# Kernel tuning notes

Hardware: AMD Instinct MI355X
Metric: run time of the kernel (lower is better)

The kernel has to match this reference:

```python
import jax, jax.numpy as jnp
import numpy as np


def setup_inputs() -> dict:
    key = jax.random.key(0)
    kx, kw = jax.random.split(key)
    x = jax.random.normal(kx, (32, 64, 112, 112), dtype=jnp.float32)
    weights = jax.random.normal(kw, (128, 64, 3, 3), dtype=jnp.float32)
    return {"x": x, "weights": weights}


def reference(x, weights):
    # The torch module's triple loop computes a standard VALID conv2d,
    # stride 1, no padding, weights shared across spatial locations.
    # x: [B, Cin, H, W]; weights: [Cout, Cin, k, k] -> out: [B, Cout, H-k+1, W-k+1]
    out = jax.lax.conv_general_dilated(
        x, weights,
        window_strides=(1, 1),
        padding="VALID",
        dimension_numbers=("NCHW", "OIHW", "NCHW"),
    )
    return out
```

## Files before the change

kernel.cpp:

```cpp
#include <hip/hip_runtime.h>


typedef short bf16x8 __attribute__((ext_vector_type(8)));
typedef float f32x4 __attribute__((ext_vector_type(4)));

__device__ __forceinline__ unsigned short f2bf(float f) {
    unsigned int u = __builtin_bit_cast(unsigned int, f);
    unsigned int r = u + 0x7fffu + ((u >> 16) & 1u);
    return (unsigned short)(r >> 16);
}
__device__ __forceinline__ unsigned int pack2(float lo, float hi) {
    return (unsigned)f2bf(lo) | ((unsigned)f2bf(hi) << 16);
}

__global__ void wperm_kernel(const float* __restrict__ W, unsigned short* __restrict__ wp) {
    int t = blockIdx.x * 256 + threadIdx.x;
    if (t < 73728) {
        int r  = t >> 13;
        int co = (t >> 6) & 127;
        int ci = t & 63;
        wp[t] = f2bf(W[(co * 64 + ci) * 9 + r]);
    }
}

__global__ __launch_bounds__(256, 2) void conv_mfma(const float* __restrict__ x,
                                                    const unsigned short* __restrict__ wp,
                                                    float* __restrict__ out) {
    __shared__ alignas(16) unsigned short xwin[324 * 72];
    __shared__ alignas(16) unsigned short wpl[128 * 72];

    const int tid  = threadIdx.x;
    const int lane = tid & 63;
    const int wv   = tid >> 6;
    const int quad = lane >> 4;
    const int l15  = lane & 15;

    const int blk  = blockIdx.x;
    const int xcd  = blk & 7;
    const int slot = blk >> 3;
    const int b    = xcd + 8 * (slot / 49);
    const int tile = slot % 49;
    const int oh0  = (tile / 7) * 16;
    const int ow0  = (tile % 7) * 16;

    const float* xb = x + b * 802816;

    const uint4* wsrc = reinterpret_cast<const uint4*>(wp) + tid * 4;
    uint4 wreg[4];
    #pragma unroll
    for (int j = 0; j < 4; j++) wreg[j] = wsrc[j];

    for (int t = tid; t < 2304; t += 256) {
        const int cgl = t & 7;
        const int hwl = (t >> 3) & 7;
        const int cgh = (t >> 6) & 3;
        const int hwh = t >> 8;
        const int cg  = cgh * 8 + cgl;
        const int hw  = hwh * 8 + hwl;
        const int hh  = hw >> 2;
        const int wc  = hw & 3;
        const int h   = min(oh0 + hh, 111);
        const float* p0 = xb + (2 * cg) * 12544 + h * 112 + ow0 + wc * 4;
        const f32x4 a = *reinterpret_cast<const f32x4*>(p0);
        const f32x4 c = *reinterpret_cast<const f32x4*>(p0 + 12544);
        unsigned int* dst = reinterpret_cast<unsigned int*>(
            &xwin[(hh * 18 + wc * 4) * 72 + 2 * cg]);
        dst[0]   = pack2(a[0], c[0]);
        dst[36]  = pack2(a[1], c[1]);
        dst[72]  = pack2(a[2], c[2]);
        dst[108] = pack2(a[3], c[3]);
    }
    for (int u = tid; u < 576; u += 256) {
        const int cg  = u & 31;
        const int hh  = u >> 5;
        const int h   = min(oh0 + hh, 111);
        const int w16 = min(ow0 + 16, 111);
        const int w17 = min(ow0 + 17, 111);
        const float* p0 = xb + (2 * cg) * 12544 + h * 112;
        unsigned int* dst = reinterpret_cast<unsigned int*>(
            &xwin[(hh * 18 + 16) * 72 + 2 * cg]);
        dst[0]  = pack2(p0[w16], p0[12544 + w16]);
        dst[36] = pack2(p0[w17], p0[12544 + w17]);
    }

    f32x4 acc[8][4];
    const f32x4 zero = {0.0f, 0.0f, 0.0f, 0.0f};
    #pragma unroll
    for (int mt = 0; mt < 8; mt++)
        #pragma unroll
        for (int nt = 0; nt < 4; nt++) acc[mt][nt] = zero;

    const int co_w   = tid >> 1;
    const int half_w = tid & 1;

    for (int r = 0; r < 9; r++) {
        const int kh = r / 3;
        const int kw = r % 3;

        __syncthreads();
        {
            uint4* dst = reinterpret_cast<uint4*>(&wpl[co_w * 72 + half_w * 32]);
            #pragma unroll
            for (int j = 0; j < 4; j++) dst[j] = wreg[j];
        }
        if (r < 8) {
            const uint4* s = wsrc + (r + 1) * 1024;
            #pragma unroll
            for (int j = 0; j < 4; j++) wreg[j] = s[j];
        }
        __syncthreads();

        #pragma unroll
        for (int cs = 0; cs < 2; cs++) {
            const int ko = cs * 32 + quad * 8;
            bf16x8 bfrag[4];
            #pragma unroll
            for (int nt = 0; nt < 4; nt++)
                bfrag[nt] = *reinterpret_cast<const bf16x8*>(
                    &xwin[((wv * 4 + nt + kh) * 18 + (l15 + kw)) * 72 + ko]);
            #pragma unroll
            for (int mt = 0; mt < 8; mt++) {
                const bf16x8 afrag = *reinterpret_cast<const bf16x8*>(
                    &wpl[(mt * 16 + l15) * 72 + ko]);
                #pragma unroll
                for (int nt = 0; nt < 4; nt++)
                    acc[mt][nt] = __builtin_amdgcn_mfma_f32_16x16x32_bf16(
                        afrag, bfrag[nt], acc[mt][nt], 0, 0, 0);
            }
        }
    }

    const int owc = ow0 + l15;
    if (owc < 110) {
        float* ob = out + b * 1548800;
        #pragma unroll
        for (int mt = 0; mt < 8; mt++) {
            #pragma unroll
            for (int nt = 0; nt < 4; nt++) {
                const int oh = oh0 + wv * 4 + nt;
                if (oh < 110) {
                    #pragma unroll
                    for (int reg = 0; reg < 4; reg++) {
                        const int co = mt * 16 + quad * 4 + reg;
                        ob[(co * 110 + oh) * 110 + owc] = acc[mt][nt][reg];
                    }
                }
            }
        }
    }
}

extern "C" void kernel_launch(void* const* d_in, const int* in_sizes, int n_in,
                              void* d_out, int out_size, void* d_ws, size_t ws_size,
                              hipStream_t stream) {
    const float* x = (const float*)d_in[0];
    const float* W = (const float*)d_in[1];
    float* out = (float*)d_out;
    unsigned short* wp = (unsigned short*)d_ws;

    wperm_kernel<<<288, 256, 0, stream>>>(W, wp);
    conv_mfma<<<32 * 49, 256, 0, stream>>>(x, wp, out);
}
```

Before: 365.7 us.

## Read MFMA weight fragments directly from global memory and split output channels across waves

```diff
diff --git a/kernel.cpp b/kernel.cpp
--- a/kernel.cpp
+++ b/kernel.cpp
@@ -16,24 +16,34 @@
 __global__ void wperm_kernel(const float* __restrict__ W, unsigned short* __restrict__ wp) {
     int t = blockIdx.x * 256 + threadIdx.x;
     if (t < 73728) {
-        int r  = t >> 13;
-        int co = (t >> 6) & 127;
-        int ci = t & 63;
+        int e    = t & 7;
+        int l15  = (t >> 3) & 15;
+        int quad = (t >> 7) & 3;
+        int cs   = (t >> 9) & 1;
+        int cog  = (t >> 10) & 7;
+        int r    = t >> 13;
+        int ci = cs * 32 + quad * 8 + e;
+        int co = cog * 16 + l15;
         wp[t] = f2bf(W[(co * 64 + ci) * 9 + r]);
     }
 }
 
-__global__ __launch_bounds__(256, 2) void conv_mfma(const float* __restrict__ x,
+__global__ __launch_bounds__(512, 4) void conv_mfma(const float* __restrict__ x,
                                                     const unsigned short* __restrict__ wp,
                                                     float* __restrict__ out) {
     __shared__ alignas(16) unsigned short xwin[324 * 72];
-    __shared__ alignas(16) unsigned short wpl[128 * 72];
 
     const int tid  = threadIdx.x;
     const int lane = tid & 63;
     const int wv   = tid >> 6;
+    const int wvoh = wv & 3;
+    const int wvco = wv >> 1 & 0;
     const int quad = lane >> 4;
     const int l15  = lane & 15;
+
+    const int wco  = wv >> 2;
+    const int woh  = wv & 3;
+    (void)wvoh; (void)wvco;
 
     const int blk  = blockIdx.x;
     const int xcd  = blk & 7;
@@ -45,12 +55,7 @@
 
     const float* xb = x + b * 802816;
 
-    const uint4* wsrc = reinterpret_cast<const uint4*>(wp) + tid * 4;
-    uint4 wreg[4];
-    #pragma unroll
-    for (int j = 0; j < 4; j++) wreg[j] = wsrc[j];
-
-    for (int t = tid; t < 2304; t += 256) {
+    for (int t = tid; t < 2304; t += 512) {
         const int cgl = t & 7;
         const int hwl = (t >> 3) & 7;
         const int cgh = (t >> 6) & 3;
@@ -70,7 +75,7 @@
         dst[72]  = pack2(a[2], c[2]);
         dst[108] = pack2(a[3], c[3]);
     }
-    for (int u = tid; u < 576; u += 256) {
+    for (int u = tid; u < 576; u += 512) {
         const int cg  = u & 31;
         const int hh  = u >> 5;
         const int h   = min(oh0 + hh, 111);
@@ -83,61 +88,53 @@
         dst[36] = pack2(p0[w17], p0[12544 + w17]);
     }
 
-    f32x4 acc[8][4];
+    f32x4 acc[4][4];
     const f32x4 zero = {0.0f, 0.0f, 0.0f, 0.0f};
     #pragma unroll
-    for (int mt = 0; mt < 8; mt++)
+    for (int mt = 0; mt < 4; mt++)
         #pragma unroll
         for (int nt = 0; nt < 4; nt++) acc[mt][nt] = zero;
 
-    const int co_w   = tid >> 1;
-    const int half_w = tid & 1;
+    __syncthreads();
 
+    const bf16x8* wq = reinterpret_cast<const bf16x8*>(wp) + lane;
+    const int cogb = wco * 4;
+
+    #pragma unroll
     for (int r = 0; r < 9; r++) {
         const int kh = r / 3;
         const int kw = r % 3;
-
-        __syncthreads();
-        {
-            uint4* dst = reinterpret_cast<uint4*>(&wpl[co_w * 72 + half_w * 32]);
-            #pragma unroll
-            for (int j = 0; j < 4; j++) dst[j] = wreg[j];
-        }
-        if (r < 8) {
-            const uint4* s = wsrc + (r + 1) * 1024;
-            #pragma unroll
-            for (int j = 0; j < 4; j++) wreg[j] = s[j];
-        }
-        __syncthreads();
-
         #pragma unroll
         for (int cs = 0; cs < 2; cs++) {
             const int ko = cs * 32 + quad * 8;
+            bf16x8 af[4];
+            #pragma unroll
+            for (int mt = 0; mt < 4; mt++)
+                af[mt] = wq[((r * 8 + cogb + mt) * 2 + cs) * 64];
             bf16x8 bfrag[4];
             #pragma unroll
             for (int nt = 0; nt < 4; nt++)
                 bfrag[nt] = *reinterpret_cast<const bf16x8*>(
-                    &xwin[((wv * 4 + nt + kh) * 18 + (l15 + kw)) * 72 + ko]);
+                    &xwin[((woh * 4 + nt + kh) * 18 + (l15 + kw)) * 72 + ko]);
+            __builtin_amdgcn_s_setprio(1);
             #pragma unroll
-            for (int mt = 0; mt < 8; mt++) {
-                const bf16x8 afrag = *reinterpret_cast<const bf16x8*>(
-                    &wpl[(mt * 16 + l15) * 72 + ko]);
+            for (int mt = 0; mt < 4; mt++)
                 #pragma unroll
                 for (int nt = 0; nt < 4; nt++)
                     acc[mt][nt] = __builtin_amdgcn_mfma_f32_16x16x32_bf16(
-                        afrag, bfrag[nt], acc[mt][nt], 0, 0, 0);
-            }
+                        af[mt], bfrag[nt], acc[mt][nt], 0, 0, 0);
+            __builtin_amdgcn_s_setprio(0);
         }
     }
 
     const int owc = ow0 + l15;
     if (owc < 110) {
-        float* ob = out + b * 1548800;
+        float* ob = out + b * 1548800 + wco * 64 * 12100;
         #pragma unroll
-        for (int mt = 0; mt < 8; mt++) {
+        for (int mt = 0; mt < 4; mt++) {
             #pragma unroll
             for (int nt = 0; nt < 4; nt++) {
-                const int oh = oh0 + wv * 4 + nt;
+                const int oh = oh0 + woh * 4 + nt;
                 if (oh < 110) {
                     #pragma unroll
                     for (int reg = 0; reg < 4; reg++) {
@@ -159,5 +156,5 @@
     unsigned short* wp = (unsigned short*)d_ws;
 
     wperm_kernel<<<288, 256, 0, stream>>>(W, wp);
-    conv_mfma<<<32 * 49, 256, 0, stream>>>(x, wp, out);
+    conv_mfma<<<32 * 49, 512, 0, stream>>>(x, wp, out);
 }
```

Measured after the change: 353.4 us. -3.4%, faster.
